# Kernel tuning notes

Hardware: AMD Instinct MI355X
Metric: run time of the kernel (lower is better)

Reference implementation:

```python
import jax, jax.numpy as jnp
import numpy as np

HIDDEN = 2048
KEY_DIM = 2048
NUM_HEADS = 16
HEAD_DIM = KEY_DIM // NUM_HEADS
ROPE_THETA = 10000.0
EPS = 1e-05


def rms_norm(x, w, eps=EPS):
    var = jnp.mean(x * x, axis=-1, keepdims=True)
    return x * jax.lax.rsqrt(var + eps) * w


def apply_rope(x, theta_base=ROPE_THETA):
    # x: [b, s, h, d]; faithful to the einops repeat '(2 d)' = tile (concat), with
    # even output positions = cos*x1 - sin*x2, odd = sin*x1 + cos*x2.
    b, s, h, d = x.shape
    half = d // 2
    freqs = theta_base ** (jnp.arange(half, dtype=x.dtype) * (-2.0 / d))  # [d/2]
    freqs = jnp.concatenate([freqs, freqs], axis=-1)                      # [d] (tiled)
    pos = jnp.arange(s, dtype=x.dtype)                                    # [s]
    ang = pos[:, None] * freqs[None, :]                                   # [s, d]
    cos = jnp.cos(ang)[None, :, None, :]
    sin = jnp.sin(ang)[None, :, None, :]
    x_even = x[..., 0::2]
    x_odd = x[..., 1::2]
    x1 = jnp.concatenate([x_even, x_even], axis=-1)  # tile '(2 d)'
    x2 = jnp.concatenate([x_odd, x_odd], axis=-1)
    even_mask = (jnp.arange(d) % 2 == 0)[None, None, None, :]
    return jnp.where(even_mask, cos * x1 - sin * x2, sin * x1 + cos * x2)


def setup_inputs() -> dict:
    key = jax.random.key(0)
    ks = jax.random.split(key, 10)
    B, S = 2, 2048
    s_in = 1.0 / np.sqrt(HIDDEN)
    s_k = 1.0 / np.sqrt(KEY_DIM)
    return {
        "x": jax.random.normal(ks[0], (B, S, HIDDEN), dtype=jnp.float32),
        "rms_w": jnp.ones((HIDDEN,), dtype=jnp.float32),
        "wq": jax.random.normal(ks[1], (HIDDEN, KEY_DIM), dtype=jnp.float32) * s_in,
        "bq": jnp.zeros((KEY_DIM,), dtype=jnp.float32),
        "wk": jax.random.normal(ks[2], (HIDDEN, KEY_DIM), dtype=jnp.float32) * s_in,
        "bk": jnp.zeros((KEY_DIM,), dtype=jnp.float32),
        "wv": jax.random.normal(ks[3], (HIDDEN, KEY_DIM), dtype=jnp.float32) * s_in,
        "bv": jnp.zeros((KEY_DIM,), dtype=jnp.float32),
        "wo": jax.random.normal(ks[4], (KEY_DIM, HIDDEN), dtype=jnp.float32) * s_k,
        "bo": jnp.zeros((HIDDEN,), dtype=jnp.float32),
    }


def reference(x, rms_w, wq, bq, wk, bk, wv, bv, wo, bo):
    B, S, _ = x.shape
    residual = x
    xn = rms_norm(x, rms_w)
    q = (xn @ wq + bq).reshape(B, S, NUM_HEADS, HEAD_DIM)
    k = (xn @ wk + bk).reshape(B, S, NUM_HEADS, HEAD_DIM)
    v = (xn @ wv + bv).reshape(B, S, NUM_HEADS, HEAD_DIM)
    q = apply_rope(q)
    k = apply_rope(k)
    scores = jnp.einsum('bshd,bthd->bhst', q, k) / jnp.sqrt(
        jnp.asarray(HEAD_DIM, dtype=x.dtype))
    causal = jnp.tril(jnp.ones((S, S), dtype=bool))[None, None]
    scores = jnp.where(causal, scores, -jnp.inf)
    probs = jax.nn.softmax(scores, axis=-1)
    out = jnp.einsum('bhst,bthd->bshd', probs, v).reshape(B, S, KEY_DIM)
    return out @ wo + bo + residual
```

## Files before the change

kernel.cpp:

```cpp
#include <hip/hip_runtime.h>
#include <stdint.h>
#include <math.h>

#define S_LEN 2048
#define HID 2048
#define NH 16
#define HD 128
#define NROWS 4096
#define SCALE 0.08838834764831845f
#define C2 (0.08838834764831845f * 1.442695040888963f)

typedef unsigned short u16;
typedef __attribute__((ext_vector_type(8))) short short8;
typedef __attribute__((ext_vector_type(4))) float f32x4;
typedef __attribute__((ext_vector_type(16))) float f32x16;
typedef __attribute__((ext_vector_type(4))) unsigned short u16x4;
typedef __attribute__((ext_vector_type(4))) unsigned int u32x4;
typedef __attribute__((ext_vector_type(4))) float float4v;

__device__ __forceinline__ u16 f2bf(float f) {
  union { float f; uint32_t u; } v; v.f = f;
  uint32_t r = v.u + 0x7FFFu + ((v.u >> 16) & 1u);
  return (u16)(r >> 16);
}
__device__ __forceinline__ float bf2f(u16 b) {
  union { uint32_t u; float f; } v; v.u = ((uint32_t)b) << 16;
  return v.f;
}
__device__ __forceinline__ void gl_lds16(const void* g, void* l) {
  __builtin_amdgcn_global_load_lds((const __attribute__((address_space(1))) void*)g,
                                   (__attribute__((address_space(3))) void*)l, 16, 0, 0);
}
__device__ __forceinline__ unsigned cvtpk(float lo, float hi) {
  unsigned r;
  asm("v_cvt_pk_bf16_f32 %0, %1, %2" : "=v"(r) : "v"(lo), "v"(hi));
  return r;
}
__device__ __forceinline__ void plswap(unsigned &a, unsigned &b) {
  asm volatile("v_permlane32_swap_b32 %0, %1" : "+v"(a), "+v"(b));
}

__global__ __launch_bounds__(256) void k_rmsnorm(const float* __restrict__ x,
                                                 const float* __restrict__ w,
                                                 u16* __restrict__ xn) {
  int row = blockIdx.x;
  int tid = threadIdx.x;
  const float* xr = x + (size_t)row * HID;
  float4v a = *(const float4v*)(xr + tid * 8);
  float4v b = *(const float4v*)(xr + tid * 8 + 4);
  float s = a[0]*a[0] + a[1]*a[1] + a[2]*a[2] + a[3]*a[3]
          + b[0]*b[0] + b[1]*b[1] + b[2]*b[2] + b[3]*b[3];
  #pragma unroll
  for (int off = 1; off < 64; off <<= 1) s += __shfl_xor(s, off, 64);
  __shared__ float red[4];
  int wv = tid >> 6;
  if ((tid & 63) == 0) red[wv] = s;
  __syncthreads();
  float tot = red[0] + red[1] + red[2] + red[3];
  float r = rsqrtf(tot * (1.0f / HID) + 1e-5f);
  const float* wp = w + tid * 8;
  u16x4 o0, o1;
  #pragma unroll
  for (int j = 0; j < 4; ++j) { o0[j] = f2bf(a[j] * r * wp[j]); o1[j] = f2bf(b[j] * r * wp[4 + j]); }
  *(u16x4*)(xn + (size_t)row * HID + tid * 8) = o0;
  *(u16x4*)(xn + (size_t)row * HID + tid * 8 + 4) = o1;
}

__global__ __launch_bounds__(256) void k_wconv4(const float* __restrict__ w0, const float* __restrict__ w1,
                                                const float* __restrict__ w2, const float* __restrict__ w3,
                                                u16* __restrict__ wtbase) {
  int z = blockIdx.z;
  const float* w = (z == 0) ? w0 : (z == 1) ? w1 : (z == 2) ? w2 : w3;
  u16* wt = wtbase + (size_t)z * HID * HID;
  int n0 = blockIdx.x * 64, k0 = blockIdx.y * 64;
  __shared__ float t[64][68];
  int tid = threadIdx.x;
  int cr = tid >> 4;
  int cc = (tid & 15) * 4;
  #pragma unroll
  for (int it = 0; it < 4; ++it) {
    int kk = cr + it * 16;
    float4v v = *(const float4v*)(w + (size_t)(k0 + kk) * HID + n0 + cc);
    t[kk][cc] = v[0]; t[kk][cc + 1] = v[1]; t[kk][cc + 2] = v[2]; t[kk][cc + 3] = v[3];
  }
  __syncthreads();
  #pragma unroll
  for (int it = 0; it < 4; ++it) {
    int nn = cr + it * 16;
    u16x4 o;
    #pragma unroll
    for (int j = 0; j < 4; ++j) o[j] = f2bf(t[cc + j][nn]);
    *(u16x4*)(wt + (size_t)(n0 + nn) * HID + k0 + cc) = o;
  }
}

__global__ __launch_bounds__(256) void k_ropepack(const u16* __restrict__ qh, const u16* __restrict__ kh,
                                                  u16* __restrict__ QP, u16* __restrict__ KP) {
  int tid = threadIdx.x;
  int l = tid & 63, wvv = tid >> 6;
  int rsub = l >> 4, c = l & 15;
  int row = blockIdx.x * 16 + wvv * 4 + rsub;
  int bh = row >> 11, s = row & 2047;
  int tile = s >> 5, ln = s & 31;
  int ks = c >> 1, hi = c & 1;
  int k3 = ks & 3;
  const u16* qi = qh + (size_t)row * HD + 32 * k3 + 16 * hi;
  const u16* ki = kh + (size_t)row * HD + 32 * k3 + 16 * hi;
  float sn[8], cs[8];
  #pragma unroll
  for (int j = 0; j < 8; ++j) {
    int de = 16 * k3 + 8 * hi + j;
    float freq = exp2f((float)de * -0.20762050593046014f);
    sincosf((float)s * freq, &sn[j], &cs[j]);
  }
  size_t off = ((((size_t)(bh * 64 + tile)) * 8 + ks) * 64 + hi * 32 + ln) * 8;
  {
    short8 a = *(const short8*)(qi);
    short8 b2 = *(const short8*)(qi + 8);
    u16x4 o0, o1;
    #pragma unroll
    for (int j = 0; j < 4; ++j) {
      float x0 = bf2f((u16)a[2 * j]), x1 = bf2f((u16)a[2 * j + 1]);
      o0[j] = f2bf((j & 1) ? (sn[j] * x0 + cs[j] * x1) : (cs[j] * x0 - sn[j] * x1));
    }
    #pragma unroll
    for (int j = 0; j < 4; ++j) {
      int jj = j + 4;
      float x0 = bf2f((u16)b2[2 * j]), x1 = bf2f((u16)b2[2 * j + 1]);
      o1[j] = f2bf((jj & 1) ? (sn[jj] * x0 + cs[jj] * x1) : (cs[jj] * x0 - sn[jj] * x1));
    }
    *(u16x4*)(QP + off) = o0; *(u16x4*)(QP + off + 4) = o1;
  }
  {
    short8 a = *(const short8*)(ki);
    short8 b2 = *(const short8*)(ki + 8);
    u16x4 o0, o1;
    #pragma unroll
    for (int j = 0; j < 4; ++j) {
      float x0 = bf2f((u16)a[2 * j]), x1 = bf2f((u16)a[2 * j + 1]);
      o0[j] = f2bf((j & 1) ? (sn[j] * x0 + cs[j] * x1) : (cs[j] * x0 - sn[j] * x1));
    }
    #pragma unroll
    for (int j = 0; j < 4; ++j) {
      int jj = j + 4;
      float x0 = bf2f((u16)b2[2 * j]), x1 = bf2f((u16)b2[2 * j + 1]);
      o1[j] = f2bf((jj & 1) ? (sn[jj] * x0 + cs[jj] * x1) : (cs[jj] * x0 - sn[jj] * x1));
    }
    *(u16x4*)(KP + off) = o0; *(u16x4*)(KP + off + 4) = o1;
  }
}

__global__ __launch_bounds__(256) void k_vpack(const u16* __restrict__ vh, u16* __restrict__ VP) {
  int bx = blockIdx.x;
  int bh = blockIdx.y;
  __shared__ u16 t[64][136];
  int tid = threadIdx.x;
  int row = tid >> 2;
  int d0 = (tid & 3) * 32;
  const u16* src = vh + ((size_t)bh * S_LEN + bx * 64 + row) * HD + d0;
  short8 a = *(const short8*)(src);
  short8 b = *(const short8*)(src + 8);
  short8 c = *(const short8*)(src + 16);
  short8 d = *(const short8*)(src + 24);
  *(short8*)(&t[row][d0]) = a;
  *(short8*)(&t[row][d0 + 8]) = b;
  *(short8*)(&t[row][d0 + 16]) = c;
  *(short8*)(&t[row][d0 + 24]) = d;
  __syncthreads();
  #pragma unroll
  for (int i = 0; i < 4; ++i) {
    int cc = i * 256 + tid;
    int lp = cc & 63;
    int db = (cc >> 6) & 3;
    int j2 = (cc >> 8) & 1;
    int tl = (cc >> 9) & 1;
    int tg = bx * 2 + tl;
    int tloc = tl * 32 + j2 * 16 + (lp >> 5) * 8;
    int dloc = db * 32 + (lp & 31);
    short8 v;
    #pragma unroll
    for (int jj = 0; jj < 8; ++jj) v[jj] = (short)t[tloc + jj][dloc];
    size_t off = ((((size_t)(bh * 64 + tg) * 2 + j2) * 4 + db) * 64 + lp) * 8;
    *(short8*)(VP + off) = v;
  }
}

__global__ __launch_bounds__(256) void k_gemm_qkv(const u16* __restrict__ A, const u16* __restrict__ BT,
                                                  const float* __restrict__ bq, const float* __restrict__ bk,
                                                  const float* __restrict__ bv, u16* __restrict__ qkv) {
  __shared__ __align__(16) u16 lA[128 * 64];
  __shared__ __align__(16) u16 lB[128 * 64];
  int bx = blockIdx.x, by = blockIdx.y;
  int sel = bx >> 4;
  const float* bias = (sel == 0) ? bq : (sel == 1) ? bk : bv;
  u16* outp = qkv + (size_t)sel * NROWS * HID;
  int tid = threadIdx.x;
  int wv = tid >> 6, lane = tid & 63;
  int wr = wv >> 1, wc = wv & 1;
  int lq = lane & 15, lg = lane >> 4;
  f32x4 acc[4][4];
  #pragma unroll
  for (int mi = 0; mi < 4; ++mi)
    #pragma unroll
    for (int ni = 0; ni < 4; ++ni) acc[mi][ni] = (f32x4){0.f, 0.f, 0.f, 0.f};

  const size_t Abase = (size_t)(by * 128) * HID;
  const size_t Bbase = (size_t)(bx * 128) * HID;
  for (int k0 = 0; k0 < HID; k0 += 64) {
    __syncthreads();
    #pragma unroll
    for (int it = 0; it < 4; ++it) {
      int c = it * 256 + tid;
      int row = c >> 3;
      int cir = (c & 7) ^ (row & 7);
      gl_lds16(A + Abase + (size_t)row * HID + k0 + cir * 8, lA + (it * 256 + wv * 64) * 8);
    }
    #pragma unroll
    for (int it = 0; it < 4; ++it) {
      int c = it * 256 + tid;
      int row = c >> 3;
      int cir = (c & 7) ^ (row & 7);
      gl_lds16(BT + Bbase + (size_t)row * HID + k0 + cir * 8, lB + (it * 256 + wv * 64) * 8);
    }
    __syncthreads();
    #pragma unroll
    for (int kk = 0; kk < 2; ++kk) {
      int ch = kk * 4 + lg;
      short8 afr[4], bfr[4];
      #pragma unroll
      for (int mi = 0; mi < 4; ++mi) {
        int r = wr * 64 + mi * 16 + lq;
        afr[mi] = *(const short8*)(lA + r * 64 + ((ch ^ (r & 7)) << 3));
      }
      #pragma unroll
      for (int ni = 0; ni < 4; ++ni) {
        int r = wc * 64 + ni * 16 + lq;
        bfr[ni] = *(const short8*)(lB + r * 64 + ((ch ^ (r & 7)) << 3));
      }
      #pragma unroll
      for (int mi = 0; mi < 4; ++mi)
        #pragma unroll
        for (int ni = 0; ni < 4; ++ni)
          acc[mi][ni] = __builtin_amdgcn_mfma_f32_16x16x32_bf16(afr[mi], bfr[ni], acc[mi][ni], 0, 0, 0);
    }
  }
  #pragma unroll
  for (int ni = 0; ni < 4; ++ni) {
    int colg = bx * 128 + wc * 64 + ni * 16 + lq;
    int col = colg & 2047;
    int h = col >> 7, d = col & 127;
    float bs = bias[col];
    #pragma unroll
    for (int mi = 0; mi < 4; ++mi) {
      #pragma unroll
      for (int r = 0; r < 4; ++r) {
        int rowm = by * 128 + wr * 64 + mi * 16 + lg * 4 + r;
        int b = rowm >> 11, s = rowm & 2047;
        outp[(((size_t)(b * NH + h)) * S_LEN + s) * HD + d] = f2bf(acc[mi][ni][r] + bs);
      }
    }
  }
}

__global__ __launch_bounds__(256) void k_gemm_o(const u16* __restrict__ A, const u16* __restrict__ BT,
                                                const float* __restrict__ bias,
                                                const float* __restrict__ resid,
                                                float* __restrict__ outp) {
  __shared__ __align__(16) u16 lA[128 * 64];
  __shared__ __align__(16) u16 lB[128 * 64];
  int bx = blockIdx.x, by = blockIdx.y;
  int tid = threadIdx.x;
  int wv = tid >> 6, lane = tid & 63;
  int wr = wv >> 1, wc = wv & 1;
  int lq = lane & 15, lg = lane >> 4;
  f32x4 acc[4][4];
  #pragma unroll
  for (int mi = 0; mi < 4; ++mi)
    #pragma unroll
    for (int ni = 0; ni < 4; ++ni) acc[mi][ni] = (f32x4){0.f, 0.f, 0.f, 0.f};

  const size_t Abase = (size_t)(by * 128) * HID;
  const size_t Bbase = (size_t)(bx * 128) * HID;
  for (int k0 = 0; k0 < HID; k0 += 64) {
    __syncthreads();
    #pragma unroll
    for (int it = 0; it < 4; ++it) {
      int c = it * 256 + tid;
      int row = c >> 3;
      int cir = (c & 7) ^ (row & 7);
      gl_lds16(A + Abase + (size_t)row * HID + k0 + cir * 8, lA + (it * 256 + wv * 64) * 8);
    }
    #pragma unroll
    for (int it = 0; it < 4; ++it) {
      int c = it * 256 + tid;
      int row = c >> 3;
      int cir = (c & 7) ^ (row & 7);
      gl_lds16(BT + Bbase + (size_t)row * HID + k0 + cir * 8, lB + (it * 256 + wv * 64) * 8);
    }
    __syncthreads();
    #pragma unroll
    for (int kk = 0; kk < 2; ++kk) {
      int ch = kk * 4 + lg;
      short8 afr[4], bfr[4];
      #pragma unroll
      for (int mi = 0; mi < 4; ++mi) {
        int r = wr * 64 + mi * 16 + lq;
        afr[mi] = *(const short8*)(lA + r * 64 + ((ch ^ (r & 7)) << 3));
      }
      #pragma unroll
      for (int ni = 0; ni < 4; ++ni) {
        int r = wc * 64 + ni * 16 + lq;
        bfr[ni] = *(const short8*)(lB + r * 64 + ((ch ^ (r & 7)) << 3));
      }
      #pragma unroll
      for (int mi = 0; mi < 4; ++mi)
        #pragma unroll
        for (int ni = 0; ni < 4; ++ni)
          acc[mi][ni] = __builtin_amdgcn_mfma_f32_16x16x32_bf16(afr[mi], bfr[ni], acc[mi][ni], 0, 0, 0);
    }
  }
  #pragma unroll
  for (int ni = 0; ni < 4; ++ni) {
    int col = bx * 128 + wc * 64 + ni * 16 + lq;
    float bs = bias[col];
    #pragma unroll
    for (int mi = 0; mi < 4; ++mi) {
      #pragma unroll
      for (int r = 0; r < 4; ++r) {
        int rowm = by * 128 + wr * 64 + mi * 16 + lg * 4 + r;
        size_t o = (size_t)rowm * HID + col;
        outp[o] = acc[mi][ni][r] + bs + resid[o];
      }
    }
  }
}

__global__ __launch_bounds__(64, 2) void k_attn(const u16* __restrict__ QP, const u16* __restrict__ KP,
                                                const u16* __restrict__ VP, u16* __restrict__ out) {
  int bid = blockIdx.x;
  int rest = bid >> 3;
  int bh = (bid & 7) * 4 + (rest & 3);
  int gg = rest >> 2;
  int qw = (gg < 32) ? (63 - gg) : (gg - 32);
  int b = bh >> 4, h = bh & 15;
  int lane = threadIdx.x;
  int hi = lane >> 5, ln = lane & 31;
  int q0 = qw * 32, qrow = q0 + ln;

  const u16* QPb = QP + ((size_t)(bh * 64 + qw) * 8) * 512 + lane * 8;
  short8 qf[8];
  #pragma unroll
  for (int ks = 0; ks < 8; ++ks) qf[ks] = *(const short8*)(QPb + ks * 512);

  f32x16 oc[4];
  #pragma unroll
  for (int db = 0; db < 4; ++db)
    #pragma unroll
    for (int r = 0; r < 16; ++r) oc[db][r] = 0.f;
  float mr = -3.0e38f, l = 0.f;

  const u16* KPb = KP + ((size_t)bh * 64 * 8) * 512 + lane * 8;
  const u16* VPb = VP + ((size_t)bh * 64 * 8) * 512 + lane * 8;

  int ntile = qw + 1;
  short8 kf[8];
  #pragma unroll
  for (int ks = 0; ks < 8; ++ks) kf[ks] = *(const short8*)(KPb + ks * 512);

  for (int tt = 0; tt < ntile; ++tt) {
    short8 va[8];
    #pragma unroll
    for (int u = 0; u < 8; ++u) va[u] = *(const short8*)(VPb + (size_t)tt * 4096 + u * 512);

    f32x16 st;
    #pragma unroll
    for (int r = 0; r < 16; ++r) st[r] = 0.f;
    __builtin_amdgcn_s_setprio(1);
    #pragma unroll
    for (int ks = 0; ks < 8; ++ks)
      st = __builtin_amdgcn_mfma_f32_32x32x16_bf16(kf[ks], qf[ks], st, 0, 0, 0);
    __builtin_amdgcn_s_setprio(0);

    if (tt + 1 < ntile) {
      #pragma unroll
      for (int ks = 0; ks < 8; ++ks)
        kf[ks] = *(const short8*)(KPb + (size_t)(tt + 1) * 4096 + ks * 512);
    }

    int t0 = tt * 32;
    float sv[16];
    float pm = -3.0e38f;
    bool lastt = (tt == ntile - 1);
    #pragma unroll
    for (int r = 0; r < 16; ++r) {
      float x = st[r];
      if (lastt) {
        int t = t0 + (r & 3) + 8 * (r >> 2) + 4 * hi;
        x = (t <= qrow) ? x : -3.0e38f;
      }
      sv[r] = x;
    }
    #pragma unroll
    for (int r = 0; r < 15; r += 2) pm = fmaxf(fmaxf(pm, sv[r]), sv[r + 1]);
    pm = fmaxf(pm, sv[15]);
    pm = fmaxf(pm, __shfl_xor(pm, 32, 64));
    if (!__all(pm <= mr + 64.0f)) {
      float mnew = fmaxf(mr, pm);
      float al = exp2f((mr - mnew) * C2);
      l *= al;
      #pragma unroll
      for (int db = 0; db < 4; ++db)
        #pragma unroll
        for (int r = 0; r < 16; ++r) oc[db][r] *= al;
      mr = mnew;
    }
    float mc = mr * C2;
    float e[16];
    float rs = 0.f;
    #pragma unroll
    for (int r = 0; r < 16; ++r) {
      e[r] = exp2f(fmaf(sv[r], C2, -mc));
      rs += e[r];
    }
    rs += __shfl_xor(rs, 32, 64);
    l += rs;

    unsigned w0 = cvtpk(e[0], e[1]),   w1 = cvtpk(e[2], e[3]);
    unsigned w2 = cvtpk(e[4], e[5]),   w3 = cvtpk(e[6], e[7]);
    unsigned w4 = cvtpk(e[8], e[9]),   w5 = cvtpk(e[10], e[11]);
    unsigned w6 = cvtpk(e[12], e[13]), w7 = cvtpk(e[14], e[15]);
    plswap(w0, w2); plswap(w1, w3); plswap(w4, w6); plswap(w5, w7);
    u32x4 pw0 = {w0, w1, w2, w3};
    u32x4 pw1 = {w4, w5, w6, w7};
    short8 pb0 = __builtin_bit_cast(short8, pw0);
    short8 pb1 = __builtin_bit_cast(short8, pw1);

    __builtin_amdgcn_s_setprio(1);
    #pragma unroll
    for (int db = 0; db < 4; ++db)
      oc[db] = __builtin_amdgcn_mfma_f32_32x32x16_bf16(va[db], pb0, oc[db], 0, 0, 0);
    #pragma unroll
    for (int db = 0; db < 4; ++db)
      oc[db] = __builtin_amdgcn_mfma_f32_32x32x16_bf16(va[4 + db], pb1, oc[db], 0, 0, 0);
    __builtin_amdgcn_s_setprio(0);
  }

  float inv = 1.0f / l;
  size_t ob = ((size_t)(b * S_LEN + qrow)) * HID + h * HD;
  #pragma unroll
  for (int db = 0; db < 4; ++db) {
    #pragma unroll
    for (int g = 0; g < 4; ++g) {
      u16x4 pk;
      #pragma unroll
      for (int j = 0; j < 4; ++j) pk[j] = f2bf(oc[db][4 * g + j] * inv);
      *(u16x4*)(out + ob + db * 32 + 8 * g + 4 * hi) = pk;
    }
  }
}

extern "C" void kernel_launch(void* const* d_in, const int* in_sizes, int n_in,
                              void* d_out, int out_size, void* d_ws, size_t ws_size,
                              hipStream_t stream) {
  const float* x    = (const float*)d_in[0];
  const float* rmsw = (const float*)d_in[1];
  const float* wq   = (const float*)d_in[2];
  const float* bq   = (const float*)d_in[3];
  const float* wk   = (const float*)d_in[4];
  const float* bk   = (const float*)d_in[5];
  const float* wv   = (const float*)d_in[6];
  const float* bv   = (const float*)d_in[7];
  const float* wo   = (const float*)d_in[8];
  const float* bo   = (const float*)d_in[9];

  char* ws = (char*)d_ws;
  const size_t SZ = (size_t)NROWS * HID * 2;
  const size_t WSZ = (size_t)HID * HID * 2;
  u16* xn   = (u16*)(ws);
  u16* wqkT = (u16*)(ws + SZ);
  u16* woT  = (u16*)(ws + SZ + 3 * WSZ);
  u16* qhm  = (u16*)(ws + SZ + 4 * WSZ);
  u16* khm  = (u16*)(ws + SZ + 4 * WSZ + SZ);
  u16* vhm  = (u16*)(ws + SZ + 4 * WSZ + 2 * SZ);
  u16* QP   = xn;
  u16* KP   = wqkT;
  u16* VP   = khm;
  u16* ao   = qhm;

  k_rmsnorm<<<dim3(NROWS), dim3(256), 0, stream>>>(x, rmsw, xn);
  k_wconv4<<<dim3(32, 32, 4), dim3(256), 0, stream>>>(wq, wk, wv, wo, wqkT);
  k_gemm_qkv<<<dim3(48, 32), dim3(256), 0, stream>>>(xn, wqkT, bq, bk, bv, qhm);
  k_ropepack<<<dim3(4096), dim3(256), 0, stream>>>(qhm, khm, QP, KP);
  k_vpack<<<dim3(32, 32), dim3(256), 0, stream>>>(vhm, VP);
  k_attn<<<dim3(2048), dim3(64), 0, stream>>>(QP, KP, VP, ao);
  k_gemm_o<<<dim3(16, 32), dim3(256), 0, stream>>>(ao, woT, bo, x, (float*)d_out);
}
```

Baseline: 279.2 us.

## Rewrite QKV and output GEMMs with 4-stage async LDS pipeline and 128x256 tiles

Replaces the single-buffered 128x128 GEMM kernels with 512-thread blocks computing 128x256 tiles. A 4-slot global-to-LDS ring with k-step 32 keeps three loads in flight, using manual vmcnt waits and a single barrier per step. The change also adds XCD-aware block index remapping and MFMA priority boosts. It aims to hide global load latency and raise MFMA utilisation, at the cost of 96KB dynamic LDS per block and fragile hand-tuned waitcnt logic. The larger tiles also cut the output GEMM grid to 256 blocks.

Result: no change. 280.9 us (+0.6%).

```diff
diff --git a/kernel.cpp b/kernel.cpp
--- a/kernel.cpp
+++ b/kernel.cpp
@@ -185,19 +185,20 @@
   }
 }
 
-__global__ __launch_bounds__(256) void k_gemm_qkv(const u16* __restrict__ A, const u16* __restrict__ BT,
-                                                  const float* __restrict__ bq, const float* __restrict__ bk,
-                                                  const float* __restrict__ bv, u16* __restrict__ qkv) {
-  __shared__ __align__(16) u16 lA[128 * 64];
-  __shared__ __align__(16) u16 lB[128 * 64];
-  int bx = blockIdx.x, by = blockIdx.y;
-  int sel = bx >> 4;
-  const float* bias = (sel == 0) ? bq : (sel == 1) ? bk : bv;
-  u16* outp = qkv + (size_t)sel * NROWS * HID;
+__global__ __launch_bounds__(512, 2) void k_gemm_qkv2(const u16* __restrict__ A, const u16* __restrict__ BT,
+                                                      const float* __restrict__ bq, const float* __restrict__ bk,
+                                                      const float* __restrict__ bv, u16* __restrict__ qkv) {
+  extern __shared__ __align__(16) char smraw[];
+  u16* sm = (u16*)smraw;
+  int bid = blockIdx.x;
+  int xcd = bid & 7, loc = bid >> 3;
+  int bx = xcd * 3 + loc % 3;
+  int by = loc / 3;
   int tid = threadIdx.x;
-  int wv = tid >> 6, lane = tid & 63;
-  int wr = wv >> 1, wc = wv & 1;
+  int w = tid >> 6, lane = tid & 63;
+  int wr = w >> 2, wc = w & 3;
   int lq = lane & 15, lg = lane >> 4;
+
   f32x4 acc[4][4];
   #pragma unroll
   for (int mi = 0; mi < 4; ++mi)
@@ -205,51 +206,63 @@
     for (int ni = 0; ni < 4; ++ni) acc[mi][ni] = (f32x4){0.f, 0.f, 0.f, 0.f};
 
   const size_t Abase = (size_t)(by * 128) * HID;
-  const size_t Bbase = (size_t)(bx * 128) * HID;
-  for (int k0 = 0; k0 < HID; k0 += 64) {
-    __syncthreads();
-    #pragma unroll
-    for (int it = 0; it < 4; ++it) {
-      int c = it * 256 + tid;
-      int row = c >> 3;
-      int cir = (c & 7) ^ (row & 7);
-      gl_lds16(A + Abase + (size_t)row * HID + k0 + cir * 8, lA + (it * 256 + wv * 64) * 8);
-    }
-    #pragma unroll
-    for (int it = 0; it < 4; ++it) {
-      int c = it * 256 + tid;
-      int row = c >> 3;
-      int cir = (c & 7) ^ (row & 7);
-      gl_lds16(BT + Bbase + (size_t)row * HID + k0 + cir * 8, lB + (it * 256 + wv * 64) * 8);
-    }
-    __syncthreads();
-    #pragma unroll
-    for (int kk = 0; kk < 2; ++kk) {
-      int ch = kk * 4 + lg;
-      short8 afr[4], bfr[4];
-      #pragma unroll
-      for (int mi = 0; mi < 4; ++mi) {
-        int r = wr * 64 + mi * 16 + lq;
-        afr[mi] = *(const short8*)(lA + r * 64 + ((ch ^ (r & 7)) << 3));
-      }
-      #pragma unroll
-      for (int ni = 0; ni < 4; ++ni) {
-        int r = wc * 64 + ni * 16 + lq;
-        bfr[ni] = *(const short8*)(lB + r * 64 + ((ch ^ (r & 7)) << 3));
-      }
-      #pragma unroll
-      for (int mi = 0; mi < 4; ++mi)
-        #pragma unroll
-        for (int ni = 0; ni < 4; ++ni)
-          acc[mi][ni] = __builtin_amdgcn_mfma_f32_16x16x32_bf16(afr[mi], bfr[ni], acc[mi][ni], 0, 0, 0);
-    }
-  }
+  const size_t Bbase = (size_t)(bx * 256) * HID;
+
+  #define STAGE_Q(n)  do { \
+    int slot_ = ((n) & 3) * 12288; \
+    int kb_ = (n) * 32; \
+    { int c_ = tid; int row_ = c_ >> 2; int ch_ = (c_ & 3) ^ (row_ & 3); \
+      gl_lds16(A + Abase + (size_t)row_ * HID + kb_ + ch_ * 8, sm + slot_ + c_ * 8); } \
+    _Pragma("unroll") \
+    for (int it_ = 0; it_ < 2; ++it_) { \
+      int c_ = it_ * 512 + tid; int row_ = c_ >> 2; int ch_ = (c_ & 3) ^ (row_ & 3); \
+      gl_lds16(BT + Bbase + (size_t)row_ * HID + kb_ + ch_ * 8, sm + slot_ + 4096 + c_ * 8); } \
+  } while (0)
+
+  STAGE_Q(0); STAGE_Q(1); STAGE_Q(2); STAGE_Q(3);
+  asm volatile("s_waitcnt vmcnt(6)" ::: "memory");
+  __builtin_amdgcn_s_barrier();
+  __builtin_amdgcn_sched_barrier(0);
+
+  for (int n = 0; n < 64; ++n) {
+    if (n >= 1 && n <= 60) STAGE_Q(n + 3);
+    int slot = (n & 3) * 12288;
+    const u16* sA = sm + slot;
+    const u16* sB = sm + slot + 4096;
+    short8 af[4], bf[4];
+    #pragma unroll
+    for (int mi = 0; mi < 4; ++mi) {
+      int ra = wr * 64 + mi * 16 + lq;
+      af[mi] = *(const short8*)(sA + ra * 32 + ((lg ^ (ra & 3)) << 3));
+    }
+    #pragma unroll
+    for (int ni = 0; ni < 4; ++ni) {
+      int rb = wc * 64 + ni * 16 + lq;
+      bf[ni] = *(const short8*)(sB + rb * 32 + ((lg ^ (rb & 3)) << 3));
+    }
+    __builtin_amdgcn_s_setprio(1);
+    #pragma unroll
+    for (int mi = 0; mi < 4; ++mi)
+      #pragma unroll
+      for (int ni = 0; ni < 4; ++ni)
+        acc[mi][ni] = __builtin_amdgcn_mfma_f32_16x16x32_bf16(af[mi], bf[ni], acc[mi][ni], 0, 0, 0);
+    __builtin_amdgcn_s_setprio(0);
+    if (n <= 60)      asm volatile("s_waitcnt vmcnt(6)" ::: "memory");
+    else if (n == 61) asm volatile("s_waitcnt vmcnt(3)" ::: "memory");
+    else              asm volatile("s_waitcnt vmcnt(0)" ::: "memory");
+    __builtin_amdgcn_s_barrier();
+    __builtin_amdgcn_sched_barrier(0);
+  }
+
   #pragma unroll
   for (int ni = 0; ni < 4; ++ni) {
-    int colg = bx * 128 + wc * 64 + ni * 16 + lq;
+    int colg = bx * 256 + wc * 64 + ni * 16 + lq;
+    int sel = colg >> 11;
     int col = colg & 2047;
     int h = col >> 7, d = col & 127;
+    const float* bias = (sel == 0) ? bq : (sel == 1) ? bk : bv;
     float bs = bias[col];
+    u16* outp = qkv + (size_t)sel * NROWS * HID;
     #pragma unroll
     for (int mi = 0; mi < 4; ++mi) {
       #pragma unroll
@@ -260,19 +273,23 @@
       }
     }
   }
-}
-
-__global__ __launch_bounds__(256) void k_gemm_o(const u16* __restrict__ A, const u16* __restrict__ BT,
-                                                const float* __restrict__ bias,
-                                                const float* __restrict__ resid,
-                                                float* __restrict__ outp) {
-  __shared__ __align__(16) u16 lA[128 * 64];
-  __shared__ __align__(16) u16 lB[128 * 64];
-  int bx = blockIdx.x, by = blockIdx.y;
+  #undef STAGE_Q
+}
+
+__global__ __launch_bounds__(512, 2) void k_gemm_o2(const u16* __restrict__ A, const u16* __restrict__ BT,
+                                                    const float* __restrict__ bias,
+                                                    const float* __restrict__ resid,
+                                                    float* __restrict__ outp) {
+  extern __shared__ __align__(16) char smraw[];
+  u16* sm = (u16*)smraw;
+  int bid = blockIdx.x;
+  int bx = bid & 7;
+  int by = bid >> 3;
   int tid = threadIdx.x;
-  int wv = tid >> 6, lane = tid & 63;
-  int wr = wv >> 1, wc = wv & 1;
+  int w = tid >> 6, lane = tid & 63;
+  int wr = w >> 2, wc = w & 3;
   int lq = lane & 15, lg = lane >> 4;
+
   f32x4 acc[4][4];
   #pragma unroll
   for (int mi = 0; mi < 4; ++mi)
@@ -280,48 +297,57 @@
     for (int ni = 0; ni < 4; ++ni) acc[mi][ni] = (f32x4){0.f, 0.f, 0.f, 0.f};
 
   const size_t Abase = (size_t)(by * 128) * HID;
-  const size_t Bbase = (size_t)(bx * 128) * HID;
-  for (int k0 = 0; k0 < HID; k0 += 64) {
-    __syncthreads();
-    #pragma unroll
-    for (int it = 0; it < 4; ++it) {
-      int c = it * 256 + tid;
-      int row = c >> 3;
-      int cir = (c & 7) ^ (row & 7);
-      gl_lds16(A + Abase + (size_t)row * HID + k0 + cir * 8, lA + (it * 256 + wv * 64) * 8);
-    }
-    #pragma unroll
-    for (int it = 0; it < 4; ++it) {
-      int c = it * 256 + tid;
-      int row = c >> 3;
-      int cir = (c & 7) ^ (row & 7);
-      gl_lds16(BT + Bbase + (size_t)row * HID + k0 + cir * 8, lB + (it * 256 + wv * 64) * 8);
-    }
-    __syncthreads();
-    #pragma unroll
-    for (int kk = 0; kk < 2; ++kk) {
-      int ch = kk * 4 + lg;
-      short8 afr[4], bfr[4];
-      #pragma unroll
-      for (int mi = 0; mi < 4; ++mi) {
-        int r = wr * 64 + mi * 16 + lq;
-        afr[mi] = *(const short8*)(lA + r * 64 + ((ch ^ (r & 7)) << 3));
-      }
-      #pragma unroll
-      for (int ni = 0; ni < 4; ++ni) {
-        int r = wc * 64 + ni * 16 + lq;
-        bfr[ni] = *(const short8*)(lB + r * 64 + ((ch ^ (r & 7)) << 3));
-      }
-      #pragma unroll
-      for (int mi = 0; mi < 4; ++mi)
-        #pragma unroll
-        for (int ni = 0; ni < 4; ++ni)
-          acc[mi][ni] = __builtin_amdgcn_mfma_f32_16x16x32_bf16(afr[mi], bfr[ni], acc[mi][ni], 0, 0, 0);
-    }
-  }
+  const size_t Bbase = (size_t)(bx * 256) * HID;
+
+  #define STAGE_O(n)  do { \
+    int slot_ = ((n) & 3) * 12288; \
+    int kb_ = (n) * 32; \
+    { int c_ = tid; int row_ = c_ >> 2; int ch_ = (c_ & 3) ^ (row_ & 3); \
+      gl_lds16(A + Abase + (size_t)row_ * HID + kb_ + ch_ * 8, sm + slot_ + c_ * 8); } \
+    _Pragma("unroll") \
+    for (int it_ = 0; it_ < 2; ++it_) { \
+      int c_ = it_ * 512 + tid; int row_ = c_ >> 2; int ch_ = (c_ & 3) ^ (row_ & 3); \
+      gl_lds16(BT + Bbase + (size_t)row_ * HID + kb_ + ch_ * 8, sm + slot_ + 4096 + c_ * 8); } \
+  } while (0)
+
+  STAGE_O(0); STAGE_O(1); STAGE_O(2); STAGE_O(3);
+  asm volatile("s_waitcnt vmcnt(6)" ::: "memory");
+  __builtin_amdgcn_s_barrier();
+  __builtin_amdgcn_sched_barrier(0);
+
+  for (int n = 0; n < 64; ++n) {
+    if (n >= 1 && n <= 60) STAGE_O(n + 3);
+    int slot = (n & 3) * 12288;
+    const u16* sA = sm + slot;
+    const u16* sB = sm + slot + 4096;
+    short8 af[4], bf[4];
+    #pragma unroll
+    for (int mi = 0; mi < 4; ++mi) {
+      int ra = wr * 64 + mi * 16 + lq;
+      af[mi] = *(const short8*)(sA + ra * 32 + ((lg ^ (ra & 3)) << 3));
+    }
+    #pragma unroll
+    for (int ni = 0; ni < 4; ++ni) {
+      int rb = wc * 64 + ni * 16 + lq;
+      bf[ni] = *(const short8*)(sB + rb * 32 + ((lg ^ (rb & 3)) << 3));
+    }
+    __builtin_amdgcn_s_setprio(1);
+    #pragma unroll
+    for (int mi = 0; mi < 4; ++mi)
+      #pragma unroll
+      for (int ni = 0; ni < 4; ++ni)
+        acc[mi][ni] = __builtin_amdgcn_mfma_f32_16x16x32_bf16(af[mi], bf[ni], acc[mi][ni], 0, 0, 0);
+    __builtin_amdgcn_s_setprio(0);
+    if (n <= 60)      asm volatile("s_waitcnt vmcnt(6)" ::: "memory");
+    else if (n == 61) asm volatile("s_waitcnt vmcnt(3)" ::: "memory");
+    else              asm volatile("s_waitcnt vmcnt(0)" ::: "memory");
+    __builtin_amdgcn_s_barrier();
+    __builtin_amdgcn_sched_barrier(0);
+  }
+
   #pragma unroll
   for (int ni = 0; ni < 4; ++ni) {
-    int col = bx * 128 + wc * 64 + ni * 16 + lq;
+    int col = bx * 256 + wc * 64 + ni * 16 + lq;
     float bs = bias[col];
     #pragma unroll
     for (int mi = 0; mi < 4; ++mi) {
@@ -333,6 +359,7 @@
       }
     }
   }
+  #undef STAGE_O
 }
 
 __global__ __launch_bounds__(64, 2) void k_attn(const u16* __restrict__ QP, const u16* __restrict__ KP,
@@ -489,9 +516,9 @@
 
   k_rmsnorm<<<dim3(NROWS), dim3(256), 0, stream>>>(x, rmsw, xn);
   k_wconv4<<<dim3(32, 32, 4), dim3(256), 0, stream>>>(wq, wk, wv, wo, wqkT);
-  k_gemm_qkv<<<dim3(48, 32), dim3(256), 0, stream>>>(xn, wqkT, bq, bk, bv, qhm);
+  k_gemm_qkv2<<<dim3(768), dim3(512), 98304, stream>>>(xn, wqkT, bq, bk, bv, qhm);
   k_ropepack<<<dim3(4096), dim3(256), 0, stream>>>(qhm, khm, QP, KP);
   k_vpack<<<dim3(32, 32), dim3(256), 0, stream>>>(vhm, VP);
   k_attn<<<dim3(2048), dim3(64), 0, stream>>>(QP, KP, VP, ao);
-  k_gemm_o<<<dim3(16, 32), dim3(256), 0, stream>>>(ao, woT, bo, x, (float*)d_out);
-}
+  k_gemm_o2<<<dim3(256), dim3(512), 98304, stream>>>(ao, woT, bo, x, (float*)d_out);
+}
```
